# Kernel tuning notes

Hardware: AMD Instinct MI355X
Metric: run time of the kernel (lower is better)

## Reference

```python
import jax, jax.numpy as jnp
import numpy as np

# Fuzzy convolution (gaussian membership, 'prod' T-norm):
# firing_r(patch) = prod_{ki,kj,c} exp(-0.5*((x-mu_{r,c})*sigma_{ki,kj,c,r})^2)
#                 = exp(-0.5 * sum_{ki,kj,c} ((x-mu)*sigma)^2)
# The quadratic expands so the whole premise stage is two VALID convolutions:
#   sum (x^2)*s2 - 2*sum x*(mu*s2) + sum (mu^2)*s2,  with s2 = sigma^2.

_DN = ('NHWC', 'HWIO', 'NHWC')

def _conv(a, k):
    return jax.lax.conv_general_dilated(a, k, window_strides=(1, 1), padding='VALID', dimension_numbers=_DN)

def _firing(x, sigma, mu):
    # x: (B,H,W,C); sigma: (kh,kw,C,R); mu: (R,C)
    s2 = sigma * sigma                              # (kh,kw,C,R)
    mu_cr = mu.T[None, None, :, :]                  # (1,1,C,R)
    quad = _conv(x * x, s2) - 2.0 * _conv(x, s2 * mu_cr)  # (B,H',W',R)
    const = jnp.sum(s2 * mu_cr * mu_cr, axis=(0, 1, 2))   # (R,)
    return jnp.exp(-0.5 * (quad + const))           # (B,H',W',R)

def setup_inputs() -> dict:
    key = jax.random.key(0)
    k1, k2, k3, k4 = jax.random.split(key, 4)
    B, H, W, C = 32, 256, 256, 32
    R, O = 8, 16
    x = jax.random.normal(k1, (B, H, W, C), dtype=jnp.float32)
    # small positive sigmas keep sum over 3*3*32 window terms O(1) so firing is not ~0
    premise_sigma = 0.1 * jax.random.uniform(k2, (3, 3, C, R), dtype=jnp.float32)
    premise_mu = jax.random.normal(k3, (R, C), dtype=jnp.float32)
    residual = jnp.full((1,), 0.01, dtype=jnp.float32)  # Constant(0.01) initializer
    consequent_bias = jax.random.normal(k4, (R + 1, O), dtype=jnp.float32)
    return {"x": x, "premise_sigma": premise_sigma, "premise_mu": premise_mu,
            "residual": residual, "consequent_bias": consequent_bias}

def reference(x, premise_sigma, premise_mu, residual, consequent_bias):
    phi = _firing(x, premise_sigma, premise_mu)                     # (B,H',W',R)
    res = jnp.broadcast_to(residual, phi.shape[:-1] + (1,))         # residual rule
    phi = jnp.concatenate([phi, res], axis=-1)                      # (B,H',W',R+1)
    phi_norm = phi / (jnp.sum(phi, axis=-1, keepdims=True) + 1e-9)  # normalized firing
    # constant-output-MF consequent combine: rules -> outputs
    return jnp.einsum('bhwr,ro->bhwo', phi_norm, consequent_bias)   # (B,H',W',O)
```

## Files before the change

kernel.cpp:

```cpp
#include <hip/hip_runtime.h>


#define CIN 32
#define HH  256
#define WW  256
#define HO  254
#define WO  254
#define BB  32
#define OO  16

#define TW 64
#define TH 7
#define LROWS 9
#define LPIX 66
#define ROWCH (LPIX * 4)
#define LDS_CHUNKS (LROWS * ROWCH)
#define STAGE_ITERS 10
#define NBAND 37
#define NTILE (4 * NBAND * BB)
#define CPX (NTILE / 8)

typedef _Float16 half8 __attribute__((ext_vector_type(8)));
typedef float f32x4 __attribute__((ext_vector_type(4)));

static __device__ __forceinline__ unsigned short f2h(float f) {
    _Float16 h = (_Float16)f;
    return *reinterpret_cast<unsigned short*>(&h);
}

static __device__ __forceinline__ half8 pack_pkrtz(const float4& a, const float4& b) {
    uint4 u;
    u.x = __builtin_bit_cast(unsigned, __builtin_amdgcn_cvt_pkrtz(a.x, a.y));
    u.y = __builtin_bit_cast(unsigned, __builtin_amdgcn_cvt_pkrtz(a.z, a.w));
    u.z = __builtin_bit_cast(unsigned, __builtin_amdgcn_cvt_pkrtz(b.x, b.y));
    u.w = __builtin_bit_cast(unsigned, __builtin_amdgcn_cvt_pkrtz(b.z, b.w));
    return __builtin_bit_cast(half8, u);
}

__global__ __launch_bounds__(256) void prep_kernel(const float* __restrict__ sigma,
                                                   const float* __restrict__ mu,
                                                   unsigned short* __restrict__ wb,
                                                   float* __restrict__ Kc) {
    const int tid = threadIdx.x;
    for (int item = tid; item < 18 * 64; item += 256) {
        const int frag = item >> 6;
        const int lane = item & 63;
        const int tap = frag >> 1, ftype = frag & 1;
        const int n = lane & 15, g = lane >> 4;
#pragma unroll
        for (int e = 0; e < 8; ++e) {
            float wgt = 0.f;
            if (n < 8) {
                const int c = g * 8 + e;
                const float sg = sigma[(tap * CIN + c) * 8 + n];
                const float s2 = sg * sg;
                wgt = ftype ? -0.5f * s2 : s2 * mu[n * CIN + c];
            }
            wb[item * 8 + e] = f2h(wgt);
        }
    }
    if (tid < 8) {
        const int r = tid;
        float k = 0.f;
        for (int item = 0; item < 9 * CIN; ++item) {
            const int c = item & 31;
            const float sg = sigma[item * 8 + r];
            const float m = mu[r * CIN + c];
            k = fmaf(sg * sg, m * m, k);
        }
        Kc[r] = -0.5f * k;
    }
}

__global__ __launch_bounds__(256, 3) void fuzzy_main(const float* __restrict__ x,
                                                     const unsigned short* __restrict__ wb,
                                                     const float* __restrict__ Kc,
                                                     const float* __restrict__ residual,
                                                     const float* __restrict__ cb,
                                                     float* __restrict__ out) {
    __shared__ __align__(16) unsigned char ldsRaw[LDS_CHUNKS * 16];
    half8* ldsH = reinterpret_cast<half8*>(ldsRaw);

    const int tid = threadIdx.x;
    const int lin  = blockIdx.x;
    const int tile = (lin & 7) * CPX + (lin >> 3);
    const int jt   = tile & 3;
    const int rest = tile >> 2;
    const int it   = rest % NBAND;
    const int b    = rest / NBAND;
    const int i0 = min(TH * it, HO - TH);
    const int j0 = min(TW * jt, WO - TW);

    const float4* xbase = reinterpret_cast<const float4*>(
        x + (((size_t)b * HH + (size_t)i0) * WW + (size_t)j0) * CIN);

    float4 va[STAGE_ITERS], vb[STAGE_ITERS];
#pragma unroll
    for (int t = 0; t < STAGE_ITERS; ++t) {
        const int f = min(tid + t * 256, LDS_CHUNKS - 1);
        const int row = f / ROWCH, rem = f - row * ROWCH;
        va[t] = xbase[(size_t)row * 2048 + 2 * rem];
        vb[t] = xbase[(size_t)row * 2048 + 2 * rem + 1];
    }
#pragma unroll
    for (int t = 0; t < STAGE_ITERS; ++t) {
        const int f = tid + t * 256;
        if (f < LDS_CHUNKS) {
            const int row = f / ROWCH, rem = f - row * ROWCH;
            const int px = rem >> 2, gg = rem & 3;
            ldsH[row * ROWCH + (px << 2) + (gg ^ (px & 3))] = pack_pkrtz(va[t], vb[t]);
        }
    }

    const int lane = tid & 63;
    const int m = lane & 15, g = lane >> 4;

    const half8* wbp = reinterpret_cast<const half8*>(wb);
    half8 Bf[18];
#pragma unroll
    for (int q = 0; q < 18; ++q) Bf[q] = wbp[q * 64 + lane];

    const float res = residual[0];
    const float4 kc4 = reinterpret_cast<const float4*>(Kc)[g & 1];
    half8 a2;
#pragma unroll
    for (int e = 0; e < 8; ++e) {
        const int r = g * 8 + e;
        const float w = cb[min(r, 8) * OO + m];
        a2[e] = (_Float16)((r <= 8) ? w : 0.f);
    }
    unsigned resw;
    { unsigned short rb = f2h(res); resw = (unsigned)rb; }

    __syncthreads();

    const int wv_ = tid >> 6;

    int bc[3];
#pragma unroll
    for (int kj = 0; kj < 3; ++kj) {
        const int p = m + kj;
        bc[kj] = (p << 2) + (g ^ (p & 3));
    }

    auto compute_row = [&](int row0) {
        f32x4 acc[4];
#pragma unroll
        for (int nt = 0; nt < 4; ++nt) acc[nt] = (f32x4){0.f, 0.f, 0.f, 0.f};

        const half8* baseS = ldsH + row0 * ROWCH;
#pragma unroll
        for (int ki = 0; ki < 3; ++ki) {
#pragma unroll
            for (int kj = 0; kj < 3; ++kj) {
                const int tap = ki * 3 + kj;
                half8 ax[4];
#pragma unroll
                for (int nt = 0; nt < 4; ++nt)
                    ax[nt] = baseS[ki * ROWCH + nt * 64 + bc[kj]];
#pragma unroll
                for (int nt = 0; nt < 4; ++nt)
                    acc[nt] = __builtin_amdgcn_mfma_f32_16x16x32_f16(Bf[2 * tap], ax[nt], acc[nt], 0, 0, 0);
#pragma unroll
                for (int nt = 0; nt < 4; ++nt) {
                    const half8 ax2 = ax[nt] * ax[nt];
                    acc[nt] = __builtin_amdgcn_mfma_f32_16x16x32_f16(Bf[2 * tap + 1], ax2, acc[nt], 0, 0, 0);
                }
            }
        }

        const size_t orow = ((size_t)b * HO + (size_t)(i0 + row0)) * WO + (size_t)j0;
#pragma unroll
        for (int nt = 0; nt < 4; ++nt) {
            float phv[4];
#pragma unroll
            for (int e = 0; e < 4; ++e) {
                const float t = __expf(acc[nt][e] + ((const float*)&kc4)[e]);
                phv[e] = (g < 2) ? t : 0.f;
            }
            const float S = (phv[0] + phv[1]) + (phv[2] + phv[3]);
            const float T = S + __shfl_xor(S, 16);
            const float denom = T + __shfl_xor(T, 32) + res + 1e-9f;
            const float inv = __builtin_amdgcn_rcpf(denom);

            const unsigned w01 = (unsigned)f2h(phv[0]) | ((unsigned)f2h(phv[1]) << 16);
            const unsigned w23 = (unsigned)f2h(phv[2]) | ((unsigned)f2h(phv[3]) << 16);
            const unsigned p01 = __shfl_xor(w01, 16);
            const unsigned p23 = __shfl_xor(w23, 16);
            uint4 bw;
            bw.x = (g == 0) ? w01 : ((g == 1) ? resw : 0u);
            bw.y = (g == 0) ? w23 : 0u;
            bw.z = (g == 0) ? p01 : 0u;
            bw.w = (g == 0) ? p23 : 0u;
            const half8 b2 = __builtin_bit_cast(half8, bw);

            f32x4 acc2 = (f32x4){0.f, 0.f, 0.f, 0.f};
            acc2 = __builtin_amdgcn_mfma_f32_16x16x32_f16(a2, b2, acc2, 0, 0, 0);

            f32x4 v;
            v[0] = acc2[0] * inv; v[1] = acc2[1] * inv;
            v[2] = acc2[2] * inv; v[3] = acc2[3] * inv;
            float* op = out + (orow + (size_t)(nt * 16 + m)) * OO + g * 4;
            __builtin_nontemporal_store(v, reinterpret_cast<f32x4*>(op));
        }
    };

    compute_row(wv_);
    if (wv_ < 3) compute_row(4 + wv_);
}

extern "C" void kernel_launch(void* const* d_in, const int* in_sizes, int n_in,
                              void* d_out, int out_size, void* d_ws, size_t ws_size,
                              hipStream_t stream) {
    const float* x     = (const float*)d_in[0];
    const float* sigma = (const float*)d_in[1];
    const float* mu    = (const float*)d_in[2];
    const float* resid = (const float*)d_in[3];
    const float* cb    = (const float*)d_in[4];
    float* outp = (float*)d_out;

    float* Kc = (float*)d_ws;
    unsigned short* wb = (unsigned short*)(Kc + 8);

    hipLaunchKernelGGL(prep_kernel, dim3(1), dim3(256), 0, stream, sigma, mu, wb, Kc);
    hipLaunchKernelGGL(fuzzy_main, dim3(NTILE), dim3(256), 0, stream,
                       x, wb, Kc, resid, cb, outp);
}
```

Measured before the change: 86.57 us.

## Split LDS staging in two phases to overlap row loads with compute

Stages only the first 6 input rows into LDS before the first compute pass. The remaining 3 rows are loaded from global memory after the first row's MFMA work and written to LDS after its epilogue, followed by a barrier before the second row pass. This is meant to hide part of the global-load latency behind MFMA and epilogue work and cut initial register pressure. The cost is an extra __syncthreads and live prefetch registers across the epilogue.

New measurement: 89.35 us. 1.03x slower.

```diff
diff --git a/kernel.cpp b/kernel.cpp
--- a/kernel.cpp
+++ b/kernel.cpp
@@ -15,7 +15,9 @@
 #define LPIX 66
 #define ROWCH (LPIX * 4)
 #define LDS_CHUNKS (LROWS * ROWCH)
-#define STAGE_ITERS 10
+#define ACH (6 * ROWCH)
+#define AIT 7
+#define BIT 4
 #define NBAND 37
 #define NTILE (4 * NBAND * BB)
 #define CPX (NTILE / 8)
@@ -94,21 +96,23 @@
     const float4* xbase = reinterpret_cast<const float4*>(
         x + (((size_t)b * HH + (size_t)i0) * WW + (size_t)j0) * CIN);
 
-    float4 va[STAGE_ITERS], vb[STAGE_ITERS];
-#pragma unroll
-    for (int t = 0; t < STAGE_ITERS; ++t) {
-        const int f = min(tid + t * 256, LDS_CHUNKS - 1);
-        const int row = f / ROWCH, rem = f - row * ROWCH;
-        va[t] = xbase[(size_t)row * 2048 + 2 * rem];
-        vb[t] = xbase[(size_t)row * 2048 + 2 * rem + 1];
-    }
-#pragma unroll
-    for (int t = 0; t < STAGE_ITERS; ++t) {
-        const int f = tid + t * 256;
-        if (f < LDS_CHUNKS) {
+    {
+        float4 va[AIT], vb[AIT];
+#pragma unroll
+        for (int t = 0; t < AIT; ++t) {
+            const int f = min(tid + t * 256, ACH - 1);
             const int row = f / ROWCH, rem = f - row * ROWCH;
-            const int px = rem >> 2, gg = rem & 3;
-            ldsH[row * ROWCH + (px << 2) + (gg ^ (px & 3))] = pack_pkrtz(va[t], vb[t]);
+            va[t] = xbase[(size_t)row * 2048 + 2 * rem];
+            vb[t] = xbase[(size_t)row * 2048 + 2 * rem + 1];
+        }
+#pragma unroll
+        for (int t = 0; t < AIT; ++t) {
+            const int f = tid + t * 256;
+            if (f < ACH) {
+                const int row = f / ROWCH, rem = f - row * ROWCH;
+                const int px = rem >> 2, gg = rem & 3;
+                ldsH[row * ROWCH + (px << 2) + (gg ^ (px & 3))] = pack_pkrtz(va[t], vb[t]);
+            }
         }
     }
 
@@ -143,11 +147,9 @@
         bc[kj] = (p << 2) + (g ^ (p & 3));
     }
 
-    auto compute_row = [&](int row0) {
-        f32x4 acc[4];
+    auto compute_mfma = [&](int row0, f32x4 (&acc)[4]) {
 #pragma unroll
         for (int nt = 0; nt < 4; ++nt) acc[nt] = (f32x4){0.f, 0.f, 0.f, 0.f};
-
         const half8* baseS = ldsH + row0 * ROWCH;
 #pragma unroll
         for (int ki = 0; ki < 3; ++ki) {
@@ -168,7 +170,9 @@
                 }
             }
         }
-
+    };
+
+    auto epilogue = [&](int row0, f32x4 (&acc)[4]) {
         const size_t orow = ((size_t)b * HO + (size_t)(i0 + row0)) * WO + (size_t)j0;
 #pragma unroll
         for (int nt = 0; nt < 4; ++nt) {
@@ -205,8 +209,36 @@
         }
     };
 
-    compute_row(wv_);
-    if (wv_ < 3) compute_row(4 + wv_);
+    f32x4 acc[4];
+    compute_mfma(wv_, acc);
+
+    float4 pa[BIT], pb[BIT];
+#pragma unroll
+    for (int t = 0; t < BIT; ++t) {
+        const int f = min(ACH + tid + t * 256, LDS_CHUNKS - 1);
+        const int row = f / ROWCH, rem = f - row * ROWCH;
+        pa[t] = xbase[(size_t)row * 2048 + 2 * rem];
+        pb[t] = xbase[(size_t)row * 2048 + 2 * rem + 1];
+    }
+
+    epilogue(wv_, acc);
+
+#pragma unroll
+    for (int t = 0; t < BIT; ++t) {
+        const int f = ACH + tid + t * 256;
+        if (f < LDS_CHUNKS) {
+            const int row = f / ROWCH, rem = f - row * ROWCH;
+            const int px = rem >> 2, gg = rem & 3;
+            ldsH[row * ROWCH + (px << 2) + (gg ^ (px & 3))] = pack_pkrtz(pa[t], pb[t]);
+        }
+    }
+
+    __syncthreads();
+
+    if (wv_ < 3) {
+        compute_mfma(4 + wv_, acc);
+        epilogue(4 + wv_, acc);
+    }
 }
 
 extern "C" void kernel_launch(void* const* d_in, const int* in_sizes, int n_in,
```
